# Optimization experiments

Hardware: AMD Instinct MI355X
Metric: run time of the kernel (lower is better)

## Reference

```python
import jax, jax.numpy as jnp
import numpy as np

# ---- larq ste_sign: forward = sign (0 -> +1), backward = clipped straight-through ----
def _sign(x):
    return jnp.where(x >= 0, jnp.ones_like(x), -jnp.ones_like(x))

@jax.custom_vjp
def ste_sign(x):
    return _sign(x)

def _ste_fwd(x):
    return _sign(x), x

def _ste_bwd(x, g):
    return (g * (jnp.abs(x) <= 1.0).astype(g.dtype),)

ste_sign.defvjp(_ste_fwd, _ste_bwd)

BN_EPS = 1e-3  # keras BatchNormalization default epsilon

def conv2d(x, w, padding):
    # x: NHWC, w: HWIO
    return jax.lax.conv_general_dilated(
        x, w, window_strides=(1, 1), padding=padding,
        dimension_numbers=('NHWC', 'HWIO', 'NHWC'))

def maxpool2(x):
    return jax.lax.reduce_window(x, -jnp.inf, jax.lax.max,
                                 (1, 2, 2, 1), (1, 2, 2, 1), 'VALID')

def batchnorm(x, mean, var, beta):
    # BatchNormalization(scale=False): gamma fixed at 1
    return (x - mean) * jax.lax.rsqrt(var + BN_EPS) + beta


def setup_inputs() -> dict:
    key = jax.random.key(0)
    ks = jax.random.split(key, 20)
    d = {}
    d['x'] = jax.random.normal(ks[0], (64, 128, 128, 3), dtype=jnp.float32)
    d['w1'] = jax.random.normal(ks[1], (3, 3, 3, 32), dtype=jnp.float32)
    d['m1'] = jax.random.normal(ks[2], (32,), dtype=jnp.float32)
    d['v1'] = jax.random.uniform(ks[3], (32,), dtype=jnp.float32)
    d['b1'] = jax.random.normal(ks[4], (32,), dtype=jnp.float32)
    d['w2'] = jax.random.normal(ks[5], (3, 3, 32, 64), dtype=jnp.float32)
    d['m2'] = jax.random.normal(ks[6], (64,), dtype=jnp.float32)
    d['v2'] = jax.random.uniform(ks[7], (64,), dtype=jnp.float32)
    d['b2'] = jax.random.normal(ks[8], (64,), dtype=jnp.float32)
    d['w3'] = jax.random.normal(ks[9], (3, 3, 64, 128), dtype=jnp.float32)
    d['m3'] = jax.random.normal(ks[10], (128,), dtype=jnp.float32)
    d['v3'] = jax.random.uniform(ks[11], (128,), dtype=jnp.float32)
    d['b3'] = jax.random.normal(ks[12], (128,), dtype=jnp.float32)
    d['w4'] = jax.random.normal(ks[13], (3, 3, 128, 256), dtype=jnp.float32)
    d['m4'] = jax.random.normal(ks[14], (256,), dtype=jnp.float32)
    d['v4'] = jax.random.uniform(ks[15], (256,), dtype=jnp.float32)
    d['b4'] = jax.random.normal(ks[16], (256,), dtype=jnp.float32)
    return d


def reference(x, w1, m1, v1, b1, w2, m2, v2, b2, w3, m3, v3, b3, w4, m4, v4, b4):
    # Stem: QuantConv2D(32,3x3,valid) with kernel quantized only (no input quantizer)
    y = conv2d(x, ste_sign(w1), 'VALID')          # [B,126,126,32]
    y = batchnorm(maxpool2(y), m1, v1, b1)        # [B,63,63,32]
    # Three binarized blocks: ste_sign(input) conv ste_sign(kernel), same padding
    for w, m, v, b in ((w2, m2, v2, b2), (w3, m3, v3, b3), (w4, m4, v4, b4)):
        y = conv2d(ste_sign(y), ste_sign(w), 'SAME')
        y = batchnorm(maxpool2(y), m, v, b)       # halves spatial dims
    return y                                      # [B,7,7,256]
```

## Files before the change

### kernel.cpp

```cpp
#include <hip/hip_runtime.h>
#include <stdint.h>

#define BN_EPS 1e-3f

template <int CIN, int COUT>
__global__ void pack_w(const float* __restrict__ w, uint32_t* __restrict__ wp) {
    const int CINW = CIN / 32;
    int idx = blockIdx.x * blockDim.x + threadIdx.x;
    int total = 9 * CINW * COUT;
    if (idx >= total) return;
    int co  = idx % COUT;
    int t2  = idx / COUT;
    int wi  = t2 % CINW;
    int tap = t2 / CINW;
    uint32_t word = 0;
#pragma unroll
    for (int b = 0; b < 32; b++) {
        float val = w[((tap * CIN) + wi * 32 + b) * COUT + co];
        word |= (uint32_t)(val < 0.f) << b;
    }
    wp[idx] = word;
}

__global__ void conv1_pool_bn_pack(const float* __restrict__ x,
                                   const float* __restrict__ w1,
                                   const float* __restrict__ m1,
                                   const float* __restrict__ v1,
                                   const float* __restrict__ b1,
                                   uint32_t* __restrict__ y1p) {
    __shared__ float wlds[864];
    for (int i = threadIdx.x; i < 864; i += blockDim.x)
        wlds[i] = (w1[i] >= 0.f) ? 1.f : -1.f;
    __syncthreads();

    int idx = blockIdx.x * blockDim.x + threadIdx.x;
    const int P = 63;
    int total = 64 * P * P;
    if (idx >= total) return;
    int pw = idx % P;
    int t  = idx / P;
    int ph = t % P;
    int n  = t / P;

    float mx[32];
#pragma unroll
    for (int c = 0; c < 32; c++) mx[c] = -INFINITY;

    for (int dy = 0; dy < 2; dy++) {
        for (int dx = 0; dx < 2; dx++) {
            int oh = 2 * ph + dy, ow = 2 * pw + dx;
            float acc[32];
#pragma unroll
            for (int c = 0; c < 32; c++) acc[c] = 0.f;
            for (int kh = 0; kh < 3; kh++) {
                for (int kw = 0; kw < 3; kw++) {
                    const float* xp = x + (((n * 128 + oh + kh) * 128) + (ow + kw)) * 3;
                    float x0 = xp[0], x1 = xp[1], x2 = xp[2];
                    const float* wl = wlds + ((kh * 3 + kw) * 3) * 32;
#pragma unroll
                    for (int c = 0; c < 32; c++) acc[c] += x0 * wl[c];
#pragma unroll
                    for (int c = 0; c < 32; c++) acc[c] += x1 * wl[32 + c];
#pragma unroll
                    for (int c = 0; c < 32; c++) acc[c] += x2 * wl[64 + c];
                }
            }
#pragma unroll
            for (int c = 0; c < 32; c++) mx[c] = fmaxf(mx[c], acc[c]);
        }
    }

    uint32_t word = 0;
#pragma unroll
    for (int c = 0; c < 32; c++) {
        float y = (mx[c] - m1[c]) * rsqrtf(v1[c] + BN_EPS) + b1[c];
        word |= (uint32_t)(y < 0.f) << c;
    }
    y1p[idx] = word;
}

__global__ void bconv2(const uint32_t* __restrict__ y1p,
                       const uint32_t* __restrict__ w2p,
                       const float* __restrict__ m, const float* __restrict__ v,
                       const float* __restrict__ b, uint2* __restrict__ y2p) {
    int wid  = (blockIdx.x * blockDim.x + threadIdx.x) >> 6;
    int lane = threadIdx.x & 63;
    int pw = wid % 31;
    int t  = wid / 31;
    int ph = t % 31;
    int n  = t / 31;

    uint32_t wq[9];
#pragma unroll
    for (int tap = 0; tap < 9; tap++) wq[tap] = w2p[tap * 64 + lane];

    int best = -1000000;
#pragma unroll
    for (int dy = 0; dy < 2; dy++) {
#pragma unroll
        for (int dx = 0; dx < 2; dx++) {
            int oh = 2 * ph + dy, ow = 2 * pw + dx;
            int acc = 0, K = 0;
            for (int kh = 0; kh < 3; kh++) {
                int ih = oh - 1 + kh;
                if (ih < 0 || ih >= 63) continue;
                for (int kw = 0; kw < 3; kw++) {
                    int iw = ow - 1 + kw;
                    if (iw < 0 || iw >= 63) continue;
                    uint32_t iv = y1p[(n * 63 + ih) * 63 + iw];
                    acc += __popc(iv ^ wq[kh * 3 + kw]);
                    K += 32;
                }
            }
            best = max(best, K - 2 * acc);
        }
    }
    float y = ((float)best - m[lane]) * rsqrtf(v[lane] + BN_EPS) + b[lane];
    unsigned long long bal = __ballot(y < 0.f);
    if (lane == 0) y2p[wid] = make_uint2((uint32_t)bal, (uint32_t)(bal >> 32));
}

__global__ void bconv3(const uint2* __restrict__ y2p,
                       const uint32_t* __restrict__ w3p,
                       const float* __restrict__ m, const float* __restrict__ v,
                       const float* __restrict__ b, uint32_t* __restrict__ y3p) {
    int gwid = (blockIdx.x * blockDim.x + threadIdx.x) >> 6;
    int lane = threadIdx.x & 63;
    int half  = gwid & 1;
    int pixel = gwid >> 1;
    int co = half * 64 + lane;
    int pw = pixel % 15;
    int t  = pixel / 15;
    int ph = t % 15;
    int n  = t / 15;

    uint32_t wq0[9], wq1[9];
#pragma unroll
    for (int tap = 0; tap < 9; tap++) {
        wq0[tap] = w3p[(tap * 2 + 0) * 128 + co];
        wq1[tap] = w3p[(tap * 2 + 1) * 128 + co];
    }

    int best = -1000000;
#pragma unroll
    for (int dy = 0; dy < 2; dy++) {
#pragma unroll
        for (int dx = 0; dx < 2; dx++) {
            int oh = 2 * ph + dy, ow = 2 * pw + dx;
            int acc = 0, K = 0;
            for (int kh = 0; kh < 3; kh++) {
                int ih = oh - 1 + kh;
                if (ih < 0 || ih >= 31) continue;
                for (int kw = 0; kw < 3; kw++) {
                    int iw = ow - 1 + kw;
                    if (iw < 0 || iw >= 31) continue;
                    uint2 iv = y2p[(n * 31 + ih) * 31 + iw];
                    int tap = kh * 3 + kw;
                    acc += __popc(iv.x ^ wq0[tap]) + __popc(iv.y ^ wq1[tap]);
                    K += 64;
                }
            }
            best = max(best, K - 2 * acc);
        }
    }
    float y = ((float)best - m[co]) * rsqrtf(v[co] + BN_EPS) + b[co];
    unsigned long long bal = __ballot(y < 0.f);
    if (lane == 0) {
        y3p[pixel * 4 + half * 2 + 0] = (uint32_t)bal;
        y3p[pixel * 4 + half * 2 + 1] = (uint32_t)(bal >> 32);
    }
}

__global__ void bconv4(const uint4* __restrict__ y3p,
                       const uint32_t* __restrict__ w4p,
                       const float* __restrict__ m, const float* __restrict__ v,
                       const float* __restrict__ b, float* __restrict__ out) {
    int pixel = blockIdx.x;
    int co = threadIdx.x;
    int pw = pixel % 7;
    int t  = pixel / 7;
    int ph = t % 7;
    int n  = t / 7;

    uint4 wq[9];
#pragma unroll
    for (int tap = 0; tap < 9; tap++) {
        wq[tap].x = w4p[(tap * 4 + 0) * 256 + co];
        wq[tap].y = w4p[(tap * 4 + 1) * 256 + co];
        wq[tap].z = w4p[(tap * 4 + 2) * 256 + co];
        wq[tap].w = w4p[(tap * 4 + 3) * 256 + co];
    }

    int best = -1000000;
#pragma unroll
    for (int dy = 0; dy < 2; dy++) {
#pragma unroll
        for (int dx = 0; dx < 2; dx++) {
            int oh = 2 * ph + dy, ow = 2 * pw + dx;
            int acc = 0, K = 0;
            for (int kh = 0; kh < 3; kh++) {
                int ih = oh - 1 + kh;
                if (ih < 0 || ih >= 15) continue;
                for (int kw = 0; kw < 3; kw++) {
                    int iw = ow - 1 + kw;
                    if (iw < 0 || iw >= 15) continue;
                    uint4 iv = y3p[(n * 15 + ih) * 15 + iw];
                    int tap = kh * 3 + kw;
                    acc += __popc(iv.x ^ wq[tap].x) + __popc(iv.y ^ wq[tap].y)
                         + __popc(iv.z ^ wq[tap].z) + __popc(iv.w ^ wq[tap].w);
                    K += 128;
                }
            }
            best = max(best, K - 2 * acc);
        }
    }
    float y = ((float)best - m[co]) * rsqrtf(v[co] + BN_EPS) + b[co];
    out[pixel * 256 + co] = y;
}

extern "C" void kernel_launch(void* const* d_in, const int* in_sizes, int n_in,
                              void* d_out, int out_size, void* d_ws, size_t ws_size,
                              hipStream_t stream) {
    const float* x  = (const float*)d_in[0];
    const float* w1 = (const float*)d_in[1];
    const float* m1 = (const float*)d_in[2];
    const float* v1 = (const float*)d_in[3];
    const float* b1 = (const float*)d_in[4];
    const float* w2 = (const float*)d_in[5];
    const float* m2 = (const float*)d_in[6];
    const float* v2 = (const float*)d_in[7];
    const float* b2 = (const float*)d_in[8];
    const float* w3 = (const float*)d_in[9];
    const float* m3 = (const float*)d_in[10];
    const float* v3 = (const float*)d_in[11];
    const float* b3 = (const float*)d_in[12];
    const float* w4 = (const float*)d_in[13];
    const float* m4 = (const float*)d_in[14];
    const float* v4 = (const float*)d_in[15];
    const float* b4 = (const float*)d_in[16];
    float* out = (float*)d_out;

    char* ws = (char*)d_ws;
    size_t off = 0;
    auto take = [&](size_t bytes) -> char* {
        char* p = ws + off;
        off += (bytes + 255) & ~(size_t)255;
        return p;
    };
    uint32_t* y1p = (uint32_t*)take((size_t)64 * 63 * 63 * 4);
    uint2*    y2p = (uint2*)take((size_t)64 * 31 * 31 * 8);
    uint32_t* y3p = (uint32_t*)take((size_t)64 * 15 * 15 * 16);
    uint32_t* w2p = (uint32_t*)take(9 * 1 * 64 * 4);
    uint32_t* w3p = (uint32_t*)take(9 * 2 * 128 * 4);
    uint32_t* w4p = (uint32_t*)take(9 * 4 * 256 * 4);

    const int TB = 256;
    pack_w<32, 64><<<(9 * 1 * 64 + TB - 1) / TB, TB, 0, stream>>>(w2, w2p);
    pack_w<64, 128><<<(9 * 2 * 128 + TB - 1) / TB, TB, 0, stream>>>(w3, w3p);
    pack_w<128, 256><<<(9 * 4 * 256 + TB - 1) / TB, TB, 0, stream>>>(w4, w4p);

    {
        int total = 64 * 63 * 63;
        conv1_pool_bn_pack<<<(total + TB - 1) / TB, TB, 0, stream>>>(
            x, w1, m1, v1, b1, y1p);
    }
    {
        int waves = 64 * 31 * 31;
        bconv2<<<waves / 4, TB, 0, stream>>>(y1p, w2p, m2, v2, b2, y2p);
    }
    {
        int waves = 64 * 15 * 15 * 2;
        bconv3<<<waves / 4, TB, 0, stream>>>(y2p, w3p, m3, v3, b3, y3p);
    }
    {
        bconv4<<<64 * 7 * 7, TB, 0, stream>>>((const uint4*)y3p, w4p, m4, v4, b4, out);
    }
}
```

Before: 199.2 us.

## Tile conv1 through shared memory and reuse input windows in binary convs

Rewrites the stem conv to stage an input tile in shared memory and split channels across wave groups, so each thread keeps far fewer accumulators and input loads are reused. The binary conv kernels now load a 4x4 input window once for interior pool cells and compute all four pooled outputs from it, falling back to the bounds-checked path only at borders. The three weight-packing kernels and the w1 sign step are merged into one launch. In exchange the code is more complex and interior/border paths can diverge within a wave.

```diff
diff --git a/kernel.cpp b/kernel.cpp
--- a/kernel.cpp
+++ b/kernel.cpp
@@ -4,135 +4,197 @@
 #define BN_EPS 1e-3f
 
 template <int CIN, int COUT>
-__global__ void pack_w(const float* __restrict__ w, uint32_t* __restrict__ wp) {
+__device__ inline void packw(const float* __restrict__ w, uint32_t* __restrict__ wp, int idx) {
     const int CINW = CIN / 32;
-    int idx = blockIdx.x * blockDim.x + threadIdx.x;
-    int total = 9 * CINW * COUT;
-    if (idx >= total) return;
-    int co  = idx % COUT;
-    int t2  = idx / COUT;
-    int wi  = t2 % CINW;
+    int co = idx % COUT;
+    int t2 = idx / COUT;
+    int wi = t2 % CINW;
     int tap = t2 / CINW;
     uint32_t word = 0;
 #pragma unroll
-    for (int b = 0; b < 32; b++) {
-        float val = w[((tap * CIN) + wi * 32 + b) * COUT + co];
-        word |= (uint32_t)(val < 0.f) << b;
+    for (int bb = 0; bb < 32; bb++) {
+        float val = w[((tap * CIN) + wi * 32 + bb) * COUT + co];
+        word |= (uint32_t)(val < 0.f) << bb;
     }
     wp[idx] = word;
 }
 
-__global__ void conv1_pool_bn_pack(const float* __restrict__ x,
-                                   const float* __restrict__ w1,
-                                   const float* __restrict__ m1,
-                                   const float* __restrict__ v1,
-                                   const float* __restrict__ b1,
-                                   uint32_t* __restrict__ y1p) {
-    __shared__ float wlds[864];
-    for (int i = threadIdx.x; i < 864; i += blockDim.x)
-        wlds[i] = (w1[i] >= 0.f) ? 1.f : -1.f;
+__global__ void pack_all(const float* __restrict__ w1, const float* __restrict__ w2,
+                         const float* __restrict__ w3, const float* __restrict__ w4,
+                         float* __restrict__ w1sg, uint32_t* __restrict__ w2p,
+                         uint32_t* __restrict__ w3p, uint32_t* __restrict__ w4p) {
+    int idx = blockIdx.x * 256 + threadIdx.x;
+    if (idx < 864) { w1sg[idx] = (w1[idx] >= 0.f) ? 1.f : -1.f; return; }
+    idx -= 864;
+    if (idx < 576) { packw<32, 64>(w2, w2p, idx); return; }
+    idx -= 576;
+    if (idx < 2304) { packw<64, 128>(w3, w3p, idx); return; }
+    idx -= 2304;
+    if (idx < 9216) { packw<128, 256>(w4, w4p, idx); return; }
+}
+
+__global__ __launch_bounds__(256) void conv1_k(const float* __restrict__ x,
+                                               const float* __restrict__ wsg,
+                                               const float* __restrict__ m1,
+                                               const float* __restrict__ v1,
+                                               const float* __restrict__ b1,
+                                               uint32_t* __restrict__ y1p) {
+    __shared__ float xt[18 * 102];
+    __shared__ uint32_t half0[128];
+
+    int tile = blockIdx.x;
+    int tx = tile & 3; int t2 = tile >> 2;
+    int ty = t2 & 7;  int n = t2 >> 3;
+    int ph0 = ty * 8, pw0 = tx * 16;
+    int r0 = 2 * ph0;
+    int cf0 = (2 * pw0) * 3;
+
+    for (int i = threadIdx.x; i < 18 * 102; i += 256) {
+        int r = i / 102, c = i % 102;
+        int gr = r0 + r, gcf = cf0 + c;
+        float vv = 0.f;
+        if (gr < 128 && gcf < 384)
+            vv = x[(size_t)(n * 128 + gr) * 384 + gcf];
+        xt[i] = vv;
+    }
     __syncthreads();
 
-    int idx = blockIdx.x * blockDim.x + threadIdx.x;
-    const int P = 63;
-    int total = 64 * P * P;
-    if (idx >= total) return;
-    int pw = idx % P;
-    int t  = idx / P;
-    int ph = t % P;
-    int n  = t / P;
-
-    float mx[32];
-#pragma unroll
-    for (int c = 0; c < 32; c++) mx[c] = -INFINITY;
-
-    for (int dy = 0; dy < 2; dy++) {
-        for (int dx = 0; dx < 2; dx++) {
-            int oh = 2 * ph + dy, ow = 2 * pw + dx;
-            float acc[32];
-#pragma unroll
-            for (int c = 0; c < 32; c++) acc[c] = 0.f;
-            for (int kh = 0; kh < 3; kh++) {
-                for (int kw = 0; kw < 3; kw++) {
-                    const float* xp = x + (((n * 128 + oh + kh) * 128) + (ow + kw)) * 3;
-                    float x0 = xp[0], x1 = xp[1], x2 = xp[2];
-                    const float* wl = wlds + ((kh * 3 + kw) * 3) * 32;
-#pragma unroll
-                    for (int c = 0; c < 32; c++) acc[c] += x0 * wl[c];
-#pragma unroll
-                    for (int c = 0; c < 32; c++) acc[c] += x1 * wl[32 + c];
-#pragma unroll
-                    for (int c = 0; c < 32; c++) acc[c] += x2 * wl[64 + c];
-                }
-            }
-#pragma unroll
-            for (int c = 0; c < 32; c++) mx[c] = fmaxf(mx[c], acc[c]);
+    int wave = threadIdx.x >> 6, lane = threadIdx.x & 63;
+    int grp = wave & 1;
+    int chunk = wave >> 1;
+    int px = lane & 15, py = (chunk << 2) + (lane >> 4);
+    int ph = ph0 + py, pw = pw0 + px;
+
+    float win[48];
+#pragma unroll
+    for (int r = 0; r < 4; r++)
+#pragma unroll
+        for (int cc = 0; cc < 12; cc++)
+            win[r * 12 + cc] = xt[(2 * py + r) * 102 + px * 6 + cc];
+
+    const float* wg = wsg + grp * 16;
+    uint32_t word = 0;
+    for (int csub = 0; csub < 4; csub++) {
+        float a[4][4];
+#pragma unroll
+        for (int j = 0; j < 4; j++)
+#pragma unroll
+            for (int p = 0; p < 4; p++) a[j][p] = 0.f;
+#pragma unroll
+        for (int kh = 0; kh < 3; kh++)
+#pragma unroll
+            for (int kw = 0; kw < 3; kw++)
+#pragma unroll
+                for (int ci = 0; ci < 3; ci++) {
+                    int tap = (kh * 3 + kw) * 3 + ci;
+                    float x00 = win[kh * 12 + kw * 3 + ci];
+                    float x01 = win[kh * 12 + (kw + 1) * 3 + ci];
+                    float x10 = win[(kh + 1) * 12 + kw * 3 + ci];
+                    float x11 = win[(kh + 1) * 12 + (kw + 1) * 3 + ci];
+#pragma unroll
+                    for (int j = 0; j < 4; j++) {
+                        float w = wg[tap * 32 + csub * 4 + j];
+                        a[j][0] += x00 * w;
+                        a[j][1] += x01 * w;
+                        a[j][2] += x10 * w;
+                        a[j][3] += x11 * w;
+                    }
+                }
+#pragma unroll
+        for (int j = 0; j < 4; j++) {
+            float mx = fmaxf(fmaxf(a[j][0], a[j][1]), fmaxf(a[j][2], a[j][3]));
+            int ch = grp * 16 + csub * 4 + j;
+            float y = (mx - m1[ch]) * rsqrtf(v1[ch] + BN_EPS) + b1[ch];
+            word |= (uint32_t)(y < 0.f) << (csub * 4 + j);
         }
     }
 
-    uint32_t word = 0;
-#pragma unroll
-    for (int c = 0; c < 32; c++) {
-        float y = (mx[c] - m1[c]) * rsqrtf(v1[c] + BN_EPS) + b1[c];
-        word |= (uint32_t)(y < 0.f) << c;
-    }
-    y1p[idx] = word;
-}
-
-__global__ void bconv2(const uint32_t* __restrict__ y1p,
-                       const uint32_t* __restrict__ w2p,
-                       const float* __restrict__ m, const float* __restrict__ v,
-                       const float* __restrict__ b, uint2* __restrict__ y2p) {
-    int wid  = (blockIdx.x * blockDim.x + threadIdx.x) >> 6;
+    int pix = chunk * 64 + lane;
+    if (grp == 0) half0[pix] = word;
+    __syncthreads();
+    if (grp == 1 && ph < 63 && pw < 63)
+        y1p[(n * 63 + ph) * 63 + pw] = half0[pix] | (word << 16);
+}
+
+__global__ __launch_bounds__(256) void bconv2(const uint32_t* __restrict__ y1p,
+                                              const uint32_t* __restrict__ w2p,
+                                              const float* __restrict__ m,
+                                              const float* __restrict__ v,
+                                              const float* __restrict__ b,
+                                              uint2* __restrict__ y2p) {
+    int wid = __builtin_amdgcn_readfirstlane(blockIdx.x * 4 + (threadIdx.x >> 6));
     int lane = threadIdx.x & 63;
     int pw = wid % 31;
-    int t  = wid / 31;
+    int t = wid / 31;
     int ph = t % 31;
-    int n  = t / 31;
+    int n = t / 31;
 
     uint32_t wq[9];
 #pragma unroll
     for (int tap = 0; tap < 9; tap++) wq[tap] = w2p[tap * 64 + lane];
 
-    int best = -1000000;
-#pragma unroll
-    for (int dy = 0; dy < 2; dy++) {
-#pragma unroll
-        for (int dx = 0; dx < 2; dx++) {
-            int oh = 2 * ph + dy, ow = 2 * pw + dx;
-            int acc = 0, K = 0;
-            for (int kh = 0; kh < 3; kh++) {
-                int ih = oh - 1 + kh;
-                if (ih < 0 || ih >= 63) continue;
-                for (int kw = 0; kw < 3; kw++) {
-                    int iw = ow - 1 + kw;
-                    if (iw < 0 || iw >= 63) continue;
-                    uint32_t iv = y1p[(n * 63 + ih) * 63 + iw];
-                    acc += __popc(iv ^ wq[kh * 3 + kw]);
-                    K += 32;
-                }
-            }
-            best = max(best, K - 2 * acc);
-        }
+    int best;
+    if (ph > 0 && pw > 0) {
+        const uint32_t* p = y1p + (n * 63 + (2 * ph - 1)) * 63 + (2 * pw - 1);
+        uint32_t win[16];
+#pragma unroll
+        for (int r = 0; r < 4; r++)
+#pragma unroll
+            for (int c = 0; c < 4; c++)
+                win[r * 4 + c] = p[r * 63 + c];
+        int a0 = 0, a1 = 0, a2 = 0, a3 = 0;
+#pragma unroll
+        for (int kh = 0; kh < 3; kh++)
+#pragma unroll
+            for (int kw = 0; kw < 3; kw++) {
+                uint32_t w = wq[kh * 3 + kw];
+                a0 += __popc(win[kh * 4 + kw] ^ w);
+                a1 += __popc(win[kh * 4 + kw + 1] ^ w);
+                a2 += __popc(win[(kh + 1) * 4 + kw] ^ w);
+                a3 += __popc(win[(kh + 1) * 4 + kw + 1] ^ w);
+            }
+        best = max(max(288 - 2 * a0, 288 - 2 * a1), max(288 - 2 * a2, 288 - 2 * a3));
+    } else {
+        best = -1000000;
+#pragma unroll
+        for (int dy = 0; dy < 2; dy++)
+#pragma unroll
+            for (int dx = 0; dx < 2; dx++) {
+                int oh = 2 * ph + dy, ow = 2 * pw + dx;
+                int acc = 0, K = 0;
+                for (int kh = 0; kh < 3; kh++) {
+                    int ih = oh - 1 + kh;
+                    if (ih < 0 || ih >= 63) continue;
+                    for (int kw = 0; kw < 3; kw++) {
+                        int iw = ow - 1 + kw;
+                        if (iw < 0 || iw >= 63) continue;
+                        acc += __popc(y1p[(n * 63 + ih) * 63 + iw] ^ wq[kh * 3 + kw]);
+                        K += 32;
+                    }
+                }
+                best = max(best, K - 2 * acc);
+            }
     }
     float y = ((float)best - m[lane]) * rsqrtf(v[lane] + BN_EPS) + b[lane];
     unsigned long long bal = __ballot(y < 0.f);
     if (lane == 0) y2p[wid] = make_uint2((uint32_t)bal, (uint32_t)(bal >> 32));
 }
 
-__global__ void bconv3(const uint2* __restrict__ y2p,
-                       const uint32_t* __restrict__ w3p,
-                       const float* __restrict__ m, const float* __restrict__ v,
-                       const float* __restrict__ b, uint32_t* __restrict__ y3p) {
-    int gwid = (blockIdx.x * blockDim.x + threadIdx.x) >> 6;
+__global__ __launch_bounds__(256) void bconv3(const uint2* __restrict__ y2p,
+                                              const uint32_t* __restrict__ w3p,
+                                              const float* __restrict__ m,
+                                              const float* __restrict__ v,
+                                              const float* __restrict__ b,
+                                              uint32_t* __restrict__ y3p) {
+    int gwid = __builtin_amdgcn_readfirstlane(blockIdx.x * 4 + (threadIdx.x >> 6));
     int lane = threadIdx.x & 63;
-    int half  = gwid & 1;
+    int half = gwid & 1;
     int pixel = gwid >> 1;
     int co = half * 64 + lane;
     int pw = pixel % 15;
-    int t  = pixel / 15;
+    int t = pixel / 15;
     int ph = t % 15;
-    int n  = t / 15;
+    int n = t / 15;
 
     uint32_t wq0[9], wq1[9];
 #pragma unroll
@@ -141,27 +203,50 @@
         wq1[tap] = w3p[(tap * 2 + 1) * 128 + co];
     }
 
-    int best = -1000000;
-#pragma unroll
-    for (int dy = 0; dy < 2; dy++) {
-#pragma unroll
-        for (int dx = 0; dx < 2; dx++) {
-            int oh = 2 * ph + dy, ow = 2 * pw + dx;
-            int acc = 0, K = 0;
-            for (int kh = 0; kh < 3; kh++) {
-                int ih = oh - 1 + kh;
-                if (ih < 0 || ih >= 31) continue;
-                for (int kw = 0; kw < 3; kw++) {
-                    int iw = ow - 1 + kw;
-                    if (iw < 0 || iw >= 31) continue;
-                    uint2 iv = y2p[(n * 31 + ih) * 31 + iw];
-                    int tap = kh * 3 + kw;
-                    acc += __popc(iv.x ^ wq0[tap]) + __popc(iv.y ^ wq1[tap]);
-                    K += 64;
-                }
-            }
-            best = max(best, K - 2 * acc);
-        }
+    int best;
+    if (ph > 0 && pw > 0) {
+        const uint2* p = y2p + (n * 31 + (2 * ph - 1)) * 31 + (2 * pw - 1);
+        uint2 win[16];
+#pragma unroll
+        for (int r = 0; r < 4; r++)
+#pragma unroll
+            for (int c = 0; c < 4; c++)
+                win[r * 4 + c] = p[r * 31 + c];
+        int a0 = 0, a1 = 0, a2 = 0, a3 = 0;
+#pragma unroll
+        for (int kh = 0; kh < 3; kh++)
+#pragma unroll
+            for (int kw = 0; kw < 3; kw++) {
+                int tap = kh * 3 + kw;
+                uint32_t u0 = wq0[tap], u1 = wq1[tap];
+                a0 += __popc(win[kh * 4 + kw].x ^ u0) + __popc(win[kh * 4 + kw].y ^ u1);
+                a1 += __popc(win[kh * 4 + kw + 1].x ^ u0) + __popc(win[kh * 4 + kw + 1].y ^ u1);
+                a2 += __popc(win[(kh + 1) * 4 + kw].x ^ u0) + __popc(win[(kh + 1) * 4 + kw].y ^ u1);
+                a3 += __popc(win[(kh + 1) * 4 + kw + 1].x ^ u0) + __popc(win[(kh + 1) * 4 + kw + 1].y ^ u1);
+            }
+        best = max(max(576 - 2 * a0, 576 - 2 * a1), max(576 - 2 * a2, 576 - 2 * a3));
+    } else {
+        best = -1000000;
+#pragma unroll
+        for (int dy = 0; dy < 2; dy++)
+#pragma unroll
+            for (int dx = 0; dx < 2; dx++) {
+                int oh = 2 * ph + dy, ow = 2 * pw + dx;
+                int acc = 0, K = 0;
+                for (int kh = 0; kh < 3; kh++) {
+                    int ih = oh - 1 + kh;
+                    if (ih < 0 || ih >= 31) continue;
+                    for (int kw = 0; kw < 3; kw++) {
+                        int iw = ow - 1 + kw;
+                        if (iw < 0 || iw >= 31) continue;
+                        uint2 iv = y2p[(n * 31 + ih) * 31 + iw];
+                        int tap = kh * 3 + kw;
+                        acc += __popc(iv.x ^ wq0[tap]) + __popc(iv.y ^ wq1[tap]);
+                        K += 64;
+                    }
+                }
+                best = max(best, K - 2 * acc);
+            }
     }
     float y = ((float)best - m[co]) * rsqrtf(v[co] + BN_EPS) + b[co];
     unsigned long long bal = __ballot(y < 0.f);
@@ -171,16 +256,19 @@
     }
 }
 
-__global__ void bconv4(const uint4* __restrict__ y3p,
-                       const uint32_t* __restrict__ w4p,
-                       const float* __restrict__ m, const float* __restrict__ v,
-                       const float* __restrict__ b, float* __restrict__ out) {
+__global__ __launch_bounds__(256) void bconv4(const uint4* __restrict__ y3p,
+                                              const uint32_t* __restrict__ w4p,
+                                              const float* __restrict__ m,
+                                              const float* __restrict__ v,
+                                              const float* __restrict__ b,
+                                              float* __restrict__ out) {
     int pixel = blockIdx.x;
-    int co = threadIdx.x;
+    int lane = threadIdx.x & 63;
+    int co = (threadIdx.x >> 6) * 64 + lane;
     int pw = pixel % 7;
-    int t  = pixel / 7;
+    int t = pixel / 7;
     int ph = t % 7;
-    int n  = t / 7;
+    int n = t / 7;
 
     uint4 wq[9];
 #pragma unroll
@@ -191,28 +279,57 @@
         wq[tap].w = w4p[(tap * 4 + 3) * 256 + co];
     }
 
-    int best = -1000000;
-#pragma unroll
-    for (int dy = 0; dy < 2; dy++) {
-#pragma unroll
-        for (int dx = 0; dx < 2; dx++) {
-            int oh = 2 * ph + dy, ow = 2 * pw + dx;
-            int acc = 0, K = 0;
-            for (int kh = 0; kh < 3; kh++) {
-                int ih = oh - 1 + kh;
-                if (ih < 0 || ih >= 15) continue;
-                for (int kw = 0; kw < 3; kw++) {
-                    int iw = ow - 1 + kw;
-                    if (iw < 0 || iw >= 15) continue;
-                    uint4 iv = y3p[(n * 15 + ih) * 15 + iw];
-                    int tap = kh * 3 + kw;
-                    acc += __popc(iv.x ^ wq[tap].x) + __popc(iv.y ^ wq[tap].y)
-                         + __popc(iv.z ^ wq[tap].z) + __popc(iv.w ^ wq[tap].w);
-                    K += 128;
-                }
-            }
-            best = max(best, K - 2 * acc);
-        }
+    int best;
+    if (ph > 0 && pw > 0) {
+        const uint4* p = y3p + (n * 15 + (2 * ph - 1)) * 15 + (2 * pw - 1);
+        int a0 = 0, a1 = 0, a2 = 0, a3 = 0;
+#pragma unroll
+        for (int r = 0; r < 4; r++)
+#pragma unroll
+            for (int c = 0; c < 4; c++) {
+                uint4 iv = p[r * 15 + c];
+#pragma unroll
+                for (int kh = 0; kh < 3; kh++) {
+                    int dy = r - kh;
+                    if (dy < 0 || dy > 1) continue;
+#pragma unroll
+                    for (int kw = 0; kw < 3; kw++) {
+                        int dx = c - kw;
+                        if (dx < 0 || dx > 1) continue;
+                        int tap = kh * 3 + kw;
+                        int pc = __popc(iv.x ^ wq[tap].x) + __popc(iv.y ^ wq[tap].y)
+                               + __popc(iv.z ^ wq[tap].z) + __popc(iv.w ^ wq[tap].w);
+                        if (dy == 0 && dx == 0) a0 += pc;
+                        else if (dy == 0) a1 += pc;
+                        else if (dx == 0) a2 += pc;
+                        else a3 += pc;
+                    }
+                }
+            }
+        best = max(max(1152 - 2 * a0, 1152 - 2 * a1), max(1152 - 2 * a2, 1152 - 2 * a3));
+    } else {
+        best = -1000000;
+#pragma unroll
+        for (int dy = 0; dy < 2; dy++)
+#pragma unroll
+            for (int dx = 0; dx < 2; dx++) {
+                int oh = 2 * ph + dy, ow = 2 * pw + dx;
+                int acc = 0, K = 0;
+                for (int kh = 0; kh < 3; kh++) {
+                    int ih = oh - 1 + kh;
+                    if (ih < 0 || ih >= 15) continue;
+                    for (int kw = 0; kw < 3; kw++) {
+                        int iw = ow - 1 + kw;
+                        if (iw < 0 || iw >= 15) continue;
+                        uint4 iv = y3p[(n * 15 + ih) * 15 + iw];
+                        int tap = kh * 3 + kw;
+                        acc += __popc(iv.x ^ wq[tap].x) + __popc(iv.y ^ wq[tap].y)
+                             + __popc(iv.z ^ wq[tap].z) + __popc(iv.w ^ wq[tap].w);
+                        K += 128;
+                    }
+                }
+                best = max(best, K - 2 * acc);
+            }
     }
     float y = ((float)best - m[co]) * rsqrtf(v[co] + BN_EPS) + b[co];
     out[pixel * 256 + co] = y;
@@ -247,32 +364,21 @@
         off += (bytes + 255) & ~(size_t)255;
         return p;
     };
-    uint32_t* y1p = (uint32_t*)take((size_t)64 * 63 * 63 * 4);
-    uint2*    y2p = (uint2*)take((size_t)64 * 31 * 31 * 8);
-    uint32_t* y3p = (uint32_t*)take((size_t)64 * 15 * 15 * 16);
-    uint32_t* w2p = (uint32_t*)take(9 * 1 * 64 * 4);
-    uint32_t* w3p = (uint32_t*)take(9 * 2 * 128 * 4);
-    uint32_t* w4p = (uint32_t*)take(9 * 4 * 256 * 4);
-
-    const int TB = 256;
-    pack_w<32, 64><<<(9 * 1 * 64 + TB - 1) / TB, TB, 0, stream>>>(w2, w2p);
-    pack_w<64, 128><<<(9 * 2 * 128 + TB - 1) / TB, TB, 0, stream>>>(w3, w3p);
-    pack_w<128, 256><<<(9 * 4 * 256 + TB - 1) / TB, TB, 0, stream>>>(w4, w4p);
-
-    {
-        int total = 64 * 63 * 63;
-        conv1_pool_bn_pack<<<(total + TB - 1) / TB, TB, 0, stream>>>(
-            x, w1, m1, v1, b1, y1p);
-    }
-    {
-        int waves = 64 * 31 * 31;
-        bconv2<<<waves / 4, TB, 0, stream>>>(y1p, w2p, m2, v2, b2, y2p);
-    }
-    {
-        int waves = 64 * 15 * 15 * 2;
-        bconv3<<<waves / 4, TB, 0, stream>>>(y2p, w3p, m3, v3, b3, y3p);
-    }
-    {
-        bconv4<<<64 * 7 * 7, TB, 0, stream>>>((const uint4*)y3p, w4p, m4, v4, b4, out);
-    }
-}
+    uint32_t* y1p  = (uint32_t*)take((size_t)64 * 63 * 63 * 4);
+    uint2*    y2p  = (uint2*)take((size_t)64 * 31 * 31 * 8);
+    uint32_t* y3p  = (uint32_t*)take((size_t)64 * 15 * 15 * 16);
+    float*    w1sg = (float*)take(864 * 4);
+    uint32_t* w2p  = (uint32_t*)take(576 * 4);
+    uint32_t* w3p  = (uint32_t*)take(2304 * 4);
+    uint32_t* w4p  = (uint32_t*)take(9216 * 4);
+
+    pack_all<<<(12960 + 255) / 256, 256, 0, stream>>>(w1, w2, w3, w4, w1sg, w2p, w3p, w4p);
+
+    conv1_k<<<64 * 32, 256, 0, stream>>>(x, w1sg, m1, v1, b1, y1p);
+
+    bconv2<<<(64 * 31 * 31) / 4, 256, 0, stream>>>(y1p, w2p, m2, v2, b2, y2p);
+
+    bconv3<<<(64 * 15 * 15 * 2) / 4, 256, 0, stream>>>(y2p, w3p, m3, v3, b3, y3p);
+
+    bconv4<<<64 * 7 * 7, 256, 0, stream>>>((const uint4*)y3p, w4p, m4, v4, b4, out);
+}
```

After: 182.2 us. 1.09x faster.
